# Optimization experiments

Measured on AMD Instinct MI355X. Metric: run time of the kernel, lower is better.

## Reference

```python
import jax, jax.numpy as jnp
import numpy as np

# Dims per init_kwargs
B, C_IN, H, W = 64, 512, 28, 28
GROWTH, BN_SIZE = 32, 4
C_MID = BN_SIZE * GROWTH  # 128
EPS = 1e-5
NUM_BITS = 8          # activation & weight quantization bits
NUM_CHUNKS = 16       # RangeBN chunking (eladhoffer quantize.py default)


def quantize(x, num_bits):
    """Uniform min/max quantize-dequantize (UniformQuantize forward)."""
    mn = x.min()
    mx = x.max()
    qmax = 2.0 ** num_bits - 1.0
    scale = jnp.maximum((mx - mn) / qmax, 1e-8)
    q = jnp.round((jnp.clip(x, mn, mx) - mn) / scale)
    return q * scale + mn


def conv2d(x, w, pad):
    return jax.lax.conv_general_dilated(
        x, w, window_strides=(1, 1), padding=[(pad, pad), (pad, pad)],
        dimension_numbers=('NCHW', 'OIHW', 'NCHW'))


def batchnorm2d(x, w, b):
    # training-mode BN: batch statistics over (N,H,W), biased variance
    mean = x.mean(axis=(0, 2, 3), keepdims=True)
    var = x.var(axis=(0, 2, 3), keepdims=True)
    xhat = (x - mean) * jax.lax.rsqrt(var + EPS)
    return xhat * w.reshape(1, -1, 1, 1) + b.reshape(1, -1, 1, 1)


def range_bn(x, w, b):
    # Range-based BN (training-mode): per-channel mean, scale from chunked min/max range
    Bx, Cx, Hx, Wx = x.shape
    y = x.transpose(1, 0, 2, 3).reshape(Cx, NUM_CHUNKS, -1)  # [C, chunks, n]
    mean_max = y.max(-1).mean(-1)   # [C]
    mean_min = y.min(-1).mean(-1)   # [C]
    mean = y.reshape(Cx, -1).mean(-1)  # [C]
    n = y.shape[-1]
    scale_fix = (0.5 * 0.35) * (1.0 + (np.pi * np.log(4.0)) ** 0.5) / ((2.0 * np.log(float(n))) ** 0.5)
    scale = 1.0 / ((mean_max - mean_min) * scale_fix + EPS)
    out = (x - mean.reshape(1, Cx, 1, 1)) * scale.reshape(1, Cx, 1, 1)
    qw = quantize(w, NUM_BITS)
    qb = quantize(b, NUM_BITS)
    return out * qw.reshape(1, Cx, 1, 1) + qb.reshape(1, Cx, 1, 1)


def setup_inputs() -> dict:
    key = jax.random.key(0)
    ks = jax.random.split(key, 7)
    x = jax.random.normal(ks[0], (B, C_IN, H, W), dtype=jnp.float32)
    bn1_w = jax.random.uniform(ks[1], (C_IN,), dtype=jnp.float32, minval=0.5, maxval=1.5)
    bn1_b = jax.random.normal(ks[2], (C_IN,), dtype=jnp.float32) * 0.1
    conv1_w = jax.random.normal(ks[3], (C_MID, C_IN, 1, 1), dtype=jnp.float32) * (2.0 / C_IN) ** 0.5
    rbn_w = jax.random.uniform(ks[4], (C_MID,), dtype=jnp.float32, minval=0.5, maxval=1.5)
    rbn_b = jax.random.normal(ks[5], (C_MID,), dtype=jnp.float32) * 0.1
    conv2_w = jax.random.normal(ks[6], (GROWTH, C_MID, 3, 3), dtype=jnp.float32) * (2.0 / (9 * C_MID)) ** 0.5
    return {"x": x, "bn1_w": bn1_w, "bn1_b": bn1_b, "conv1_w": conv1_w,
            "rbn_w": rbn_w, "rbn_b": rbn_b, "conv2_w": conv2_w}


def reference(x, bn1_w, bn1_b, conv1_w, rbn_w, rbn_b, conv2_w):
    # norm1 -> relu1 -> QConv2d(1x1) -> RangeBN -> relu2 -> QConv2d(3x3) -> concat
    h = jax.nn.relu(batchnorm2d(x, bn1_w, bn1_b))
    h = conv2d(quantize(h, NUM_BITS), quantize(conv1_w, NUM_BITS), pad=0)
    h = jax.nn.relu(range_bn(h, rbn_w, rbn_b))
    h = conv2d(quantize(h, NUM_BITS), quantize(conv2_w, NUM_BITS), pad=1)
    # drop_rate = 0 -> dropout is identity
    return jnp.concatenate([x, h], axis=1)
```

## Files before the change

### kernel.cpp

```cpp
#include <hip/hip_runtime.h>
#include <math.h>

static constexpr int BB    = 64;
static constexpr int C_IN  = 512;
static constexpr int C_MID = 128;
static constexpr int C_OUT = 32;
static constexpr int C_TOT = 544;
static constexpr int HW    = 784;

static constexpr size_t H2_OFF    = 0;
static constexpr size_t QW1_OFF   = 6422528;
static constexpr size_t QW2_OFF   = QW1_OFF + 65536;
static constexpr size_t PSTAT_OFF = QW2_OFF + 49152;
static constexpr size_t BNA_OFF   = PSTAT_OFF + 16384;
static constexpr size_t BNB_OFF   = BNA_OFF + 512;
static constexpr size_t CMAX_OFF  = BNB_OFF + 512;
static constexpr size_t CMIN_OFF  = CMAX_OFF + 2048;
static constexpr size_t CSUM_OFF  = CMIN_OFF + 2048;
static constexpr size_t A2_OFF    = CSUM_OFF + 2048;
static constexpr size_t B2_OFF    = A2_OFF + 128;
static constexpr size_t QRW_OFF   = B2_OFF + 128;
static constexpr size_t QRB_OFF   = QRW_OFF + 128;
static constexpr size_t SCAL_OFF  = QRB_OFF + 128;
static constexpr size_t PART_OFF  = SCAL_OFF + 16;

#define DEVFN __device__ __forceinline__

typedef __bf16 bf16x8 __attribute__((ext_vector_type(8)));
typedef float  f32x4  __attribute__((ext_vector_type(4)));

DEVFN float qact(float v, float mn, float mx, float inv, float sc) {
    v = fminf(fmaxf(v, mn), mx);
    return fmaf(rintf((v - mn) * inv), sc, mn);
}

DEVFN unsigned f2bf(float f) {
    unsigned u = __float_as_uint(f);
    return (u + 0x7fffu + ((u >> 16) & 1u)) >> 16;
}

__global__ __launch_bounds__(256) void k_stats_copy(const float* __restrict__ x,
                                                    float* __restrict__ out,
                                                    float* __restrict__ ws) {
    const int c = blockIdx.x, bg = blockIdx.y, tid = threadIdx.x;
    float s = 0.f, s2 = 0.f, mn = INFINITY, mx = -INFINITY;
    for (int i = tid; i < 8 * 196; i += 256) {
        const int b = bg * 8 + i / 196, j = i % 196;
        const float4 v = ((const float4*)(x + ((size_t)b * C_IN + c) * HW))[j];
        ((float4*)(out + ((size_t)b * C_TOT + c) * HW))[j] = v;
        s  += (v.x + v.y) + (v.z + v.w);
        s2 += v.x * v.x + v.y * v.y + v.z * v.z + v.w * v.w;
        mn = fminf(mn, fminf(fminf(v.x, v.y), fminf(v.z, v.w)));
        mx = fmaxf(mx, fmaxf(fmaxf(v.x, v.y), fmaxf(v.z, v.w)));
    }
    __shared__ float r0[256], r1[256], r2[256], r3[256];
    r0[tid] = s; r1[tid] = s2; r2[tid] = mn; r3[tid] = mx;
    __syncthreads();
    for (int off = 128; off > 0; off >>= 1) {
        if (tid < off) {
            r0[tid] += r0[tid + off];
            r1[tid] += r1[tid + off];
            r2[tid] = fminf(r2[tid], r2[tid + off]);
            r3[tid] = fmaxf(r3[tid], r3[tid + off]);
        }
        __syncthreads();
    }
    if (tid == 0) {
        float* p = ws + PSTAT_OFF + ((size_t)c * 8 + bg) * 4;
        p[0] = r0[0]; p[1] = r1[0]; p[2] = r2[0]; p[3] = r3[0];
    }
}

__global__ __launch_bounds__(256) void k_prep_red(const float* __restrict__ conv1_w,
                                                  const float* __restrict__ conv2_w,
                                                  const float* __restrict__ bn1_w,
                                                  const float* __restrict__ bn1_b,
                                                  float* __restrict__ ws) {
    const int b = blockIdx.x, tid = threadIdx.x;
    __shared__ float ra[256], rb[256];
    float mn = INFINITY, mx = -INFINITY;

    if (b < 32) {
        const float4* src = (const float4*)conv1_w + (size_t)b * 512;
        for (int i = tid; i < 512; i += 256) {
            const float4 v = src[i];
            mn = fminf(mn, fminf(fminf(v.x, v.y), fminf(v.z, v.w)));
            mx = fmaxf(mx, fmaxf(fmaxf(v.x, v.y), fmaxf(v.z, v.w)));
        }
    } else if (b < 40) {
        const float4* src = (const float4*)conv2_w + (size_t)(b - 32) * 1152;
        for (int i = tid; i < 1152; i += 256) {
            const float4 v = src[i];
            mn = fminf(mn, fminf(fminf(v.x, v.y), fminf(v.z, v.w)));
            mx = fmaxf(mx, fmaxf(fmaxf(v.x, v.y), fmaxf(v.z, v.w)));
        }
    } else {
        if (tid < 128) {
            const int c = (b - 40) * 128 + tid;
            const float* p = ws + PSTAT_OFF + (size_t)c * 32;
            float s = 0.f, s2 = 0.f, cmn = INFINITY, cmx = -INFINITY;
            for (int g = 0; g < 8; ++g) {
                s += p[g * 4 + 0]; s2 += p[g * 4 + 1];
                cmn = fminf(cmn, p[g * 4 + 2]); cmx = fmaxf(cmx, p[g * 4 + 3]);
            }
            const float n = 50176.f;
            const float mean = s / n;
            const float var  = s2 / n - mean * mean;
            const float rstd = rsqrtf(var + 1e-5f);
            const float A  = rstd * bn1_w[c];
            const float Bc = bn1_b[c] - mean * A;
            ws[BNA_OFF + c] = A; ws[BNB_OFF + c] = Bc;
            const float v1 = A * cmn + Bc, v2 = A * cmx + Bc;
            mn = fmaxf(0.f, fminf(v1, v2));
            mx = fmaxf(0.f, fmaxf(v1, v2));
        }
    }
    ra[tid] = mn; rb[tid] = mx;
    __syncthreads();
    for (int off = 128; off > 0; off >>= 1) {
        if (tid < off) { ra[tid] = fminf(ra[tid], ra[tid + off]); rb[tid] = fmaxf(rb[tid], rb[tid + off]); }
        __syncthreads();
    }
    if (tid == 0) {
        float* p;
        if (b < 32)       p = ws + PART_OFF + (size_t)b * 2;
        else if (b < 40)  p = ws + PART_OFF + 64 + (size_t)(b - 32) * 2;
        else              p = ws + PART_OFF + 80 + (size_t)(b - 40) * 2;
        p[0] = ra[0]; p[1] = rb[0];
    }
}

__global__ __launch_bounds__(256) void k_prep_fin(const float* __restrict__ rbn_w,
                                                  const float* __restrict__ rbn_b,
                                                  float* __restrict__ ws) {
    const int tid = threadIdx.x;
    __shared__ float ra[256], rb[256];
    __shared__ float s_mn, s_sc;

    ra[tid] = tid < 32 ? ws[PART_OFF + tid * 2] : INFINITY;
    rb[tid] = tid < 32 ? ws[PART_OFF + tid * 2 + 1] : -INFINITY;
    __syncthreads();
    for (int off = 128; off > 0; off >>= 1) {
        if (tid < off) { ra[tid] = fminf(ra[tid], ra[tid + off]); rb[tid] = fmaxf(rb[tid], rb[tid + off]); }
        __syncthreads();
    }
    if (tid == 0) {
        ws[SCAL_OFF + 8] = ra[0];
        ws[SCAL_OFF + 9] = fmaxf((rb[0] - ra[0]) / 255.f, 1e-8f);
    }
    __syncthreads();

    ra[tid] = tid < 8 ? ws[PART_OFF + 64 + tid * 2] : INFINITY;
    rb[tid] = tid < 8 ? ws[PART_OFF + 64 + tid * 2 + 1] : -INFINITY;
    __syncthreads();
    for (int off = 128; off > 0; off >>= 1) {
        if (tid < off) { ra[tid] = fminf(ra[tid], ra[tid + off]); rb[tid] = fmaxf(rb[tid], rb[tid + off]); }
        __syncthreads();
    }
    if (tid == 0) {
        ws[SCAL_OFF + 10] = ra[0];
        ws[SCAL_OFF + 11] = fmaxf((rb[0] - ra[0]) / 255.f, 1e-8f);
    }
    __syncthreads();

    ra[tid] = tid < 4 ? ws[PART_OFF + 80 + tid * 2] : INFINITY;
    rb[tid] = tid < 4 ? ws[PART_OFF + 80 + tid * 2 + 1] : -INFINITY;
    __syncthreads();
    for (int off = 128; off > 0; off >>= 1) {
        if (tid < off) { ra[tid] = fminf(ra[tid], ra[tid + off]); rb[tid] = fmaxf(rb[tid], rb[tid + off]); }
        __syncthreads();
    }
    if (tid == 0) {
        const float mn1 = ra[0], mx1 = rb[0];
        const float sc = fmaxf((mx1 - mn1) / 255.f, 1e-8f);
        ws[SCAL_OFF + 0] = mn1; ws[SCAL_OFF + 1] = sc; ws[SCAL_OFF + 2] = 1.f / sc; ws[SCAL_OFF + 6] = mx1;
    }
    __syncthreads();

    for (int which = 0; which < 2; ++which) {
        const float* src = which ? rbn_b : rbn_w;
        const size_t dst = which ? QRB_OFF : QRW_OFF;
        float v = 0.f;
        ra[tid] = INFINITY; rb[tid] = -INFINITY;
        if (tid < 128) { v = src[tid]; ra[tid] = v; rb[tid] = v; }
        __syncthreads();
        for (int off = 128; off > 0; off >>= 1) {
            if (tid < off) { ra[tid] = fminf(ra[tid], ra[tid + off]); rb[tid] = fmaxf(rb[tid], rb[tid + off]); }
            __syncthreads();
        }
        if (tid == 0) { s_mn = ra[0]; s_sc = fmaxf((rb[0] - ra[0]) / 255.f, 1e-8f); }
        __syncthreads();
        if (tid < 128) ws[dst + tid] = fmaf(rintf((v - s_mn) / s_sc), s_sc, s_mn);
        __syncthreads();
    }
}

__global__ __launch_bounds__(256) void k_prep_quant(const float* __restrict__ conv1_w,
                                                    const float* __restrict__ conv2_w,
                                                    float* __restrict__ ws) {
    const int b = blockIdx.x, tid = threadIdx.x;
    if (b < 32) {
        const float mnw = ws[SCAL_OFF + 8], scw = ws[SCAL_OFF + 9];
        unsigned short* qw = (unsigned short*)(ws + QW1_OFF);
        const int base = b * 2048;
#pragma unroll
        for (int t = 0; t < 8; ++t) {
            const int i = base + t * 256 + tid;
            const int co = i >> 9, k = i & 511;
            const float v = conv1_w[i];
            const float qv = fmaf(rintf((v - mnw) / scw), scw, mnw);
            const int ks = k >> 6, kc = (k >> 3) & 7, klo = k & 7;
            qw[(((size_t)ks * 128 + co) << 6) + (((kc ^ (co & 7)) << 3) | klo)] = (unsigned short)f2bf(qv);
        }
    } else {
        const float mnw = ws[SCAL_OFF + 10], scw = ws[SCAL_OFF + 11];
        unsigned short* qw2 = (unsigned short*)(ws + QW2_OFF);
        const int base = (b - 32) * 4608;
        for (int i2 = tid; i2 < 4608; i2 += 256) {
            const int i = base + i2;
            const int co = i / 1152, r = i % 1152, ci = r / 9, tap = r % 9;
            const float v = conv2_w[i];
            const float qv = fmaf(rintf((v - mnw) / scw), scw, mnw);
            qw2[(size_t)co * 1152 + tap * 128 + ci] = (unsigned short)f2bf(qv);
        }
    }
}

__global__ __launch_bounds__(256, 2) void k_conv1(const float* __restrict__ x, float* __restrict__ ws) {
    __shared__ __align__(16) unsigned short wt[128 * 64];
    __shared__ __align__(16) unsigned short ht[112 * 64];
    const int tid = threadIdx.x;
    const int pt = blockIdx.x, b = blockIdx.y;
    const int p0 = pt * 112;
    const float mn1 = ws[SCAL_OFF + 0], sc1 = ws[SCAL_OFF + 1];
    const float inv1 = ws[SCAL_OFF + 2], mx1 = ws[SCAL_OFF + 6];
    const unsigned short* qw1 = (const unsigned short*)(ws + QW1_OFF);
    const float* xb = x + (size_t)b * C_IN * HW;

    const int o = tid & 7, q = tid >> 3;
    const int wv = tid >> 6, g = (tid >> 4) & 3, r4 = tid & 15;

    f32x4 acc[2][7];
#pragma unroll
    for (int i = 0; i < 2; ++i)
#pragma unroll
        for (int j = 0; j < 7; ++j) acc[i][j] = f32x4{0.f, 0.f, 0.f, 0.f};

    for (int ks = 0; ks < 8; ++ks) {
        const float4* wsrc = (const float4*)(qw1 + (size_t)ks * 8192);
        float4* wdst = (float4*)wt;
#pragma unroll
        for (int i = 0; i < 4; ++i) wdst[tid + i * 256] = wsrc[tid + i * 256];

        if (tid < 224) {
            const int ci0 = ks * 64 + o * 8;
            float vv[8][4];
#pragma unroll
            for (int j = 0; j < 8; ++j) {
                const float4 v = *(const float4*)(xb + (size_t)(ci0 + j) * HW + p0 + q * 4);
                const float A = ws[BNA_OFF + ci0 + j], Bc = ws[BNB_OFF + ci0 + j];
                vv[j][0] = qact(fmaxf(0.f, fmaf(v.x, A, Bc)), mn1, mx1, inv1, sc1);
                vv[j][1] = qact(fmaxf(0.f, fmaf(v.y, A, Bc)), mn1, mx1, inv1, sc1);
                vv[j][2] = qact(fmaxf(0.f, fmaf(v.z, A, Bc)), mn1, mx1, inv1, sc1);
                vv[j][3] = qact(fmaxf(0.f, fmaf(v.w, A, Bc)), mn1, mx1, inv1, sc1);
            }
#pragma unroll
            for (int r = 0; r < 4; ++r) {
                const int p = q * 4 + r;
                uint4 pk;
                pk.x = f2bf(vv[0][r]) | (f2bf(vv[1][r]) << 16);
                pk.y = f2bf(vv[2][r]) | (f2bf(vv[3][r]) << 16);
                pk.z = f2bf(vv[4][r]) | (f2bf(vv[5][r]) << 16);
                pk.w = f2bf(vv[6][r]) | (f2bf(vv[7][r]) << 16);
                *(uint4*)&ht[p * 64 + ((o ^ (p & 7)) << 3)] = pk;
            }
        }
        __syncthreads();

#pragma unroll
        for (int ksub = 0; ksub < 2; ++ksub) {
            const int kk = ksub * 4 + g;
            bf16x8 af[2], bfr[7];
#pragma unroll
            for (int ct = 0; ct < 2; ++ct) {
                const int co = wv * 32 + ct * 16 + r4;
                af[ct] = *(const bf16x8*)&wt[co * 64 + ((kk ^ (co & 7)) << 3)];
            }
#pragma unroll
            for (int pf = 0; pf < 7; ++pf) {
                const int p = pf * 16 + r4;
                bfr[pf] = *(const bf16x8*)&ht[p * 64 + ((kk ^ (p & 7)) << 3)];
            }
#pragma unroll
            for (int ct = 0; ct < 2; ++ct)
#pragma unroll
                for (int pf = 0; pf < 7; ++pf)
                    acc[ct][pf] = __builtin_amdgcn_mfma_f32_16x16x32_bf16(af[ct], bfr[pf], acc[ct][pf], 0, 0, 0);
        }
        __syncthreads();
    }

    float* hb = ws + H2_OFF + (size_t)b * C_MID * HW;
#pragma unroll
    for (int ct = 0; ct < 2; ++ct) {
        const int co0 = wv * 32 + ct * 16 + g * 4;
#pragma unroll
        for (int pf = 0; pf < 7; ++pf) {
            const int p = p0 + pf * 16 + r4;
#pragma unroll
            for (int r = 0; r < 4; ++r)
                hb[(size_t)(co0 + r) * HW + p] = acc[ct][pf][r];
        }
    }
}

__global__ __launch_bounds__(256) void k_rbn_stats(float* __restrict__ ws) {
    const int c = blockIdx.x, ch = blockIdx.y, tid = threadIdx.x;
    float s = 0.f, mn = INFINITY, mx = -INFINITY;
    for (int i = tid; i < 784; i += 256) {
        const int b = ch * 4 + i / 196, j = i % 196;
        const float4 v = ((const float4*)(ws + H2_OFF + ((size_t)b * C_MID + c) * HW))[j];
        s += (v.x + v.y) + (v.z + v.w);
        mn = fminf(mn, fminf(fminf(v.x, v.y), fminf(v.z, v.w)));
        mx = fmaxf(mx, fmaxf(fmaxf(v.x, v.y), fmaxf(v.z, v.w)));
    }
    __shared__ float r0[256], r1[256], r2[256];
    r0[tid] = s; r1[tid] = mn; r2[tid] = mx;
    __syncthreads();
    for (int off = 128; off > 0; off >>= 1) {
        if (tid < off) {
            r0[tid] += r0[tid + off];
            r1[tid] = fminf(r1[tid], r1[tid + off]);
            r2[tid] = fmaxf(r2[tid], r2[tid + off]);
        }
        __syncthreads();
    }
    if (tid == 0) {
        ws[CSUM_OFF + (size_t)c * 16 + ch] = r0[0];
        ws[CMIN_OFF + (size_t)c * 16 + ch] = r1[0];
        ws[CMAX_OFF + (size_t)c * 16 + ch] = r2[0];
    }
}

__global__ __launch_bounds__(256) void k_prep2(float* __restrict__ ws) {
    const int tid = threadIdx.x;
    __shared__ float ra[256], rb[256];
    float lo = INFINITY, hi = -INFINITY;
    if (tid < 128) {
        const int c = tid;
        float mm = 0.f, mnm = 0.f, s = 0.f, cmx = -INFINITY, cmn = INFINITY;
        for (int ch = 0; ch < 16; ++ch) {
            const float a = ws[CMAX_OFF + (size_t)c * 16 + ch];
            const float m = ws[CMIN_OFF + (size_t)c * 16 + ch];
            mm += a; mnm += m; s += ws[CSUM_OFF + (size_t)c * 16 + ch];
            cmx = fmaxf(cmx, a); cmn = fminf(cmn, m);
        }
        mm *= (1.f / 16.f); mnm *= (1.f / 16.f);
        const float mean = s / 50176.f;
        const double PI_D = 3.14159265358979323846;
        const double sfd = 0.175 * (1.0 + sqrt(PI_D * log(4.0))) / sqrt(2.0 * log(3136.0));
        const float scale = 1.f / ((mm - mnm) * (float)sfd + 1e-5f);
        const float A  = scale * ws[QRW_OFF + c];
        const float Bc = ws[QRB_OFF + c] - mean * A;
        ws[A2_OFF + c] = A; ws[B2_OFF + c] = Bc;
        const float v1 = A * cmn + Bc, v2 = A * cmx + Bc;
        lo = fmaxf(0.f, fminf(v1, v2));
        hi = fmaxf(0.f, fmaxf(v1, v2));
    }
    ra[tid] = lo; rb[tid] = hi;
    __syncthreads();
    for (int off = 128; off > 0; off >>= 1) {
        if (tid < off) { ra[tid] = fminf(ra[tid], ra[tid + off]); rb[tid] = fmaxf(rb[tid], rb[tid + off]); }
        __syncthreads();
    }
    if (tid == 0) {
        const float mn3 = ra[0], mx3 = rb[0];
        const float sc = fmaxf((mx3 - mn3) / 255.f, 1e-8f);
        ws[SCAL_OFF + 3] = mn3; ws[SCAL_OFF + 4] = sc; ws[SCAL_OFF + 5] = 1.f / sc; ws[SCAL_OFF + 7] = mx3;
    }
}

__global__ __launch_bounds__(128) void k_conv2(float* __restrict__ out, const float* __restrict__ ws) {
    __shared__ __align__(16) unsigned short lact[7 * 30 * 128];
    const int tid = threadIdx.x;
    const int pt = blockIdx.x, b = blockIdx.y;
    const int y0 = pt * 4;
    const float mn3 = ws[SCAL_OFF + 3], sc3 = ws[SCAL_OFF + 4];
    const float inv3 = ws[SCAL_OFF + 5], mx3 = ws[SCAL_OFF + 7];

    {
        const uint4 z = {0u, 0u, 0u, 0u};
        uint4* lp = (uint4*)lact;
        for (int i = tid; i < 3360; i += 128) lp[i] = z;
    }
    __syncthreads();

    const float* h2b = ws + H2_OFF + (size_t)b * C_MID * HW;
    for (int task = tid; task < 672; task += 128) {
        const int oct = task / 42, rem = task % 42, r = rem / 7, xq = rem % 7;
        const int gy = y0 - 1 + r;
        if (gy < 0 || gy > 27) continue;
        float vv[8][4];
#pragma unroll
        for (int j = 0; j < 8; ++j) {
            const int ci = oct * 8 + j;
            const float4 v = *(const float4*)(h2b + (size_t)ci * HW + gy * 28 + xq * 4);
            const float A = ws[A2_OFF + ci], Bc = ws[B2_OFF + ci];
            vv[j][0] = qact(fmaxf(0.f, fmaf(v.x, A, Bc)), mn3, mx3, inv3, sc3);
            vv[j][1] = qact(fmaxf(0.f, fmaf(v.y, A, Bc)), mn3, mx3, inv3, sc3);
            vv[j][2] = qact(fmaxf(0.f, fmaf(v.z, A, Bc)), mn3, mx3, inv3, sc3);
            vv[j][3] = qact(fmaxf(0.f, fmaf(v.w, A, Bc)), mn3, mx3, inv3, sc3);
        }
#pragma unroll
        for (int xi = 0; xi < 4; ++xi) {
            const int col = xq * 4 + xi + 1;
            const int phys = (oct + col) & 15;
            uint4 pk;
            pk.x = f2bf(vv[0][xi]) | (f2bf(vv[1][xi]) << 16);
            pk.y = f2bf(vv[2][xi]) | (f2bf(vv[3][xi]) << 16);
            pk.z = f2bf(vv[4][xi]) | (f2bf(vv[5][xi]) << 16);
            pk.w = f2bf(vv[6][xi]) | (f2bf(vv[7][xi]) << 16);
            *(uint4*)&lact[((r * 30 + col) * 16 + phys) * 8] = pk;
        }
    }
    __syncthreads();

    const int wv = tid >> 6, lane = tid & 63, r4 = lane & 15, g = lane >> 4;
    int py[4], px[4];
#pragma unroll
    for (int i = 0; i < 4; ++i) {
        const int p = (wv * 4 + i) * 16 + r4;
        py[i] = p / 28; px[i] = p % 28;
    }
    f32x4 acc[2][4];
#pragma unroll
    for (int ct = 0; ct < 2; ++ct)
#pragma unroll
        for (int i = 0; i < 4; ++i) acc[ct][i] = f32x4{0.f, 0.f, 0.f, 0.f};

    const unsigned short* qw2 = (const unsigned short*)(ws + QW2_OFF);
    for (int tap = 0; tap < 9; ++tap) {
        const int dy = tap / 3, dx = tap % 3;
        bf16x8 afr[2][4];
#pragma unroll
        for (int ct = 0; ct < 2; ++ct)
#pragma unroll
            for (int c4 = 0; c4 < 4; ++c4) {
                const int co = ct * 16 + r4;
                afr[ct][c4] = *(const bf16x8*)&qw2[(size_t)co * 1152 + tap * 128 + c4 * 32 + g * 8];
            }
#pragma unroll
        for (int c4 = 0; c4 < 4; ++c4) {
            bf16x8 bfr[4];
#pragma unroll
            for (int i = 0; i < 4; ++i) {
                const int row = py[i] + dy, col = px[i] + dx;
                const int phys = (c4 * 4 + g + col) & 15;
                bfr[i] = *(const bf16x8*)&lact[((row * 30 + col) * 16 + phys) * 8];
            }
#pragma unroll
            for (int ct = 0; ct < 2; ++ct)
#pragma unroll
                for (int i = 0; i < 4; ++i)
                    acc[ct][i] = __builtin_amdgcn_mfma_f32_16x16x32_bf16(afr[ct][c4], bfr[i], acc[ct][i], 0, 0, 0);
        }
    }

#pragma unroll
    for (int ct = 0; ct < 2; ++ct)
#pragma unroll
        for (int i = 0; i < 4; ++i) {
            const int pf = wv * 4 + i;
            if (pf < 7) {
                const int p = pf * 16 + r4;
#pragma unroll
                for (int r = 0; r < 4; ++r) {
                    const int co = ct * 16 + g * 4 + r;
                    out[((size_t)b * C_TOT + 512 + co) * HW + y0 * 28 + p] = acc[ct][i][r];
                }
            }
        }
}

extern "C" void kernel_launch(void* const* d_in, const int* in_sizes, int n_in,
                              void* d_out, int out_size, void* d_ws, size_t ws_size,
                              hipStream_t stream) {
    const float* x       = (const float*)d_in[0];
    const float* bn1_w   = (const float*)d_in[1];
    const float* bn1_b   = (const float*)d_in[2];
    const float* conv1_w = (const float*)d_in[3];
    const float* rbn_w   = (const float*)d_in[4];
    const float* rbn_b   = (const float*)d_in[5];
    const float* conv2_w = (const float*)d_in[6];
    float* out = (float*)d_out;
    float* ws  = (float*)d_ws;

    k_stats_copy<<<dim3(512, 8), 256, 0, stream>>>(x, out, ws);
    k_prep_red<<<44, 256, 0, stream>>>(conv1_w, conv2_w, bn1_w, bn1_b, ws);
    k_prep_fin<<<1, 256, 0, stream>>>(rbn_w, rbn_b, ws);
    k_prep_quant<<<40, 256, 0, stream>>>(conv1_w, conv2_w, ws);
    k_conv1<<<dim3(7, 64), 256, 0, stream>>>(x, ws);
    k_rbn_stats<<<dim3(128, 16), 256, 0, stream>>>(ws);
    k_prep2<<<1, 256, 0, stream>>>(ws);
    k_conv2<<<dim3(7, 64), 128, 0, stream>>>(out, ws);
}
```

Measured before the change: 111.7 us.

## Fuse passthrough copy and RangeBN stats into conv1 epilogue

```diff
diff --git a/kernel.cpp b/kernel.cpp
--- a/kernel.cpp
+++ b/kernel.cpp
@@ -23,6 +23,8 @@
 static constexpr size_t QRB_OFF   = QRW_OFF + 128;
 static constexpr size_t SCAL_OFF  = QRB_OFF + 128;
 static constexpr size_t PART_OFF  = SCAL_OFF + 16;
+static constexpr size_t RP_OFF    = PART_OFF + 128;
+static constexpr size_t PART2_OFF = RP_OFF + 172032;
 
 #define DEVFN __device__ __forceinline__
 
@@ -39,19 +41,21 @@
     return (u + 0x7fffu + ((u >> 16) & 1u)) >> 16;
 }
 
-__global__ __launch_bounds__(256) void k_stats_copy(const float* __restrict__ x,
-                                                    float* __restrict__ out,
-                                                    float* __restrict__ ws) {
+__global__ __launch_bounds__(256) void k_stats(const float* __restrict__ x,
+                                               float* __restrict__ ws) {
     const int c = blockIdx.x, bg = blockIdx.y, tid = threadIdx.x;
     float s = 0.f, s2 = 0.f, mn = INFINITY, mx = -INFINITY;
-    for (int i = tid; i < 8 * 196; i += 256) {
-        const int b = bg * 8 + i / 196, j = i % 196;
-        const float4 v = ((const float4*)(x + ((size_t)b * C_IN + c) * HW))[j];
-        ((float4*)(out + ((size_t)b * C_TOT + c) * HW))[j] = v;
-        s  += (v.x + v.y) + (v.z + v.w);
-        s2 += v.x * v.x + v.y * v.y + v.z * v.z + v.w * v.w;
-        mn = fminf(mn, fminf(fminf(v.x, v.y), fminf(v.z, v.w)));
-        mx = fmaxf(mx, fmaxf(fmaxf(v.x, v.y), fmaxf(v.z, v.w)));
+    if (tid < 224) {
+#pragma unroll
+        for (int k = 0; k < 7; ++k) {
+            const int idx = k * 224 + tid;
+            const int b = bg * 8 + idx / 196, j = idx % 196;
+            const float4 v = ((const float4*)(x + ((size_t)b * C_IN + c) * HW))[j];
+            s  += (v.x + v.y) + (v.z + v.w);
+            s2 += v.x * v.x + v.y * v.y + v.z * v.z + v.w * v.w;
+            mn = fminf(mn, fminf(fminf(v.x, v.y), fminf(v.z, v.w)));
+            mx = fmaxf(mx, fmaxf(fmaxf(v.x, v.y), fmaxf(v.z, v.w)));
+        }
     }
     __shared__ float r0[256], r1[256], r2[256], r3[256];
     r0[tid] = s; r1[tid] = s2; r2[tid] = mn; r3[tid] = mx;
@@ -226,7 +230,9 @@
     }
 }
 
-__global__ __launch_bounds__(256, 2) void k_conv1(const float* __restrict__ x, float* __restrict__ ws) {
+__global__ __launch_bounds__(256, 2) void k_conv1(const float* __restrict__ x,
+                                                  float* __restrict__ out,
+                                                  float* __restrict__ ws) {
     __shared__ __align__(16) unsigned short wt[128 * 64];
     __shared__ __align__(16) unsigned short ht[112 * 64];
     const int tid = threadIdx.x;
@@ -236,6 +242,7 @@
     const float inv1 = ws[SCAL_OFF + 2], mx1 = ws[SCAL_OFF + 6];
     const unsigned short* qw1 = (const unsigned short*)(ws + QW1_OFF);
     const float* xb = x + (size_t)b * C_IN * HW;
+    float* outb = out + (size_t)b * C_TOT * HW;
 
     const int o = tid & 7, q = tid >> 3;
     const int wv = tid >> 6, g = (tid >> 4) & 3, r4 = tid & 15;
@@ -257,7 +264,8 @@
             float vv[8][4];
 #pragma unroll
             for (int j = 0; j < 8; ++j) {
-                const float4 v = *(const float4*)(xb + (size_t)(ci0 + j) * HW + p0 + q * 4);
+                const f32x4 v = *(const f32x4*)(xb + (size_t)(ci0 + j) * HW + p0 + q * 4);
+                __builtin_nontemporal_store(v, (f32x4*)(outb + (size_t)(ci0 + j) * HW + p0 + q * 4));
                 const float A = ws[BNA_OFF + ci0 + j], Bc = ws[BNB_OFF + ci0 + j];
                 vv[j][0] = qact(fmaxf(0.f, fmaf(v.x, A, Bc)), mn1, mx1, inv1, sc1);
                 vv[j][1] = qact(fmaxf(0.f, fmaf(v.y, A, Bc)), mn1, mx1, inv1, sc1);
@@ -312,71 +320,85 @@
                 hb[(size_t)(co0 + r) * HW + p] = acc[ct][pf][r];
         }
     }
-}
-
-__global__ __launch_bounds__(256) void k_rbn_stats(float* __restrict__ ws) {
-    const int c = blockIdx.x, ch = blockIdx.y, tid = threadIdx.x;
+
+#pragma unroll
+    for (int ct = 0; ct < 2; ++ct)
+#pragma unroll
+        for (int r = 0; r < 4; ++r) {
+            float s = 0.f, mn = INFINITY, mx = -INFINITY;
+#pragma unroll
+            for (int pf = 0; pf < 7; ++pf) {
+                const float v = acc[ct][pf][r];
+                s += v; mn = fminf(mn, v); mx = fmaxf(mx, v);
+            }
+#pragma unroll
+            for (int m = 1; m < 16; m <<= 1) {
+                s  += __shfl_xor(s, m, 64);
+                mn  = fminf(mn, __shfl_xor(mn, m, 64));
+                mx  = fmaxf(mx, __shfl_xor(mx, m, 64));
+            }
+            if (r4 == 0) {
+                const int co = wv * 32 + ct * 16 + g * 4 + r;
+                float* dst = ws + RP_OFF + (((size_t)co * 64 + b) * 7 + pt) * 3;
+                dst[0] = s; dst[1] = mn; dst[2] = mx;
+            }
+        }
+}
+
+__global__ __launch_bounds__(64) void k_rbn_combine(float* __restrict__ ws) {
+    const int c = blockIdx.x, t = threadIdx.x;
+    const int ch = t >> 2, sub = t & 3;
+    const int b = ch * 4 + sub;
+    const float* rp = ws + RP_OFF + ((size_t)c * 64 + b) * 21;
     float s = 0.f, mn = INFINITY, mx = -INFINITY;
-    for (int i = tid; i < 784; i += 256) {
-        const int b = ch * 4 + i / 196, j = i % 196;
-        const float4 v = ((const float4*)(ws + H2_OFF + ((size_t)b * C_MID + c) * HW))[j];
-        s += (v.x + v.y) + (v.z + v.w);
-        mn = fminf(mn, fminf(fminf(v.x, v.y), fminf(v.z, v.w)));
-        mx = fmaxf(mx, fmaxf(fmaxf(v.x, v.y), fmaxf(v.z, v.w)));
-    }
-    __shared__ float r0[256], r1[256], r2[256];
-    r0[tid] = s; r1[tid] = mn; r2[tid] = mx;
-    __syncthreads();
-    for (int off = 128; off > 0; off >>= 1) {
-        if (tid < off) {
-            r0[tid] += r0[tid + off];
-            r1[tid] = fminf(r1[tid], r1[tid + off]);
-            r2[tid] = fmaxf(r2[tid], r2[tid + off]);
-        }
-        __syncthreads();
-    }
-    if (tid == 0) {
-        ws[CSUM_OFF + (size_t)c * 16 + ch] = r0[0];
-        ws[CMIN_OFF + (size_t)c * 16 + ch] = r1[0];
-        ws[CMAX_OFF + (size_t)c * 16 + ch] = r2[0];
-    }
-}
-
-__global__ __launch_bounds__(256) void k_prep2(float* __restrict__ ws) {
-    const int tid = threadIdx.x;
-    __shared__ float ra[256], rb[256];
-    float lo = INFINITY, hi = -INFINITY;
-    if (tid < 128) {
-        const int c = tid;
-        float mm = 0.f, mnm = 0.f, s = 0.f, cmx = -INFINITY, cmn = INFINITY;
-        for (int ch = 0; ch < 16; ++ch) {
-            const float a = ws[CMAX_OFF + (size_t)c * 16 + ch];
-            const float m = ws[CMIN_OFF + (size_t)c * 16 + ch];
-            mm += a; mnm += m; s += ws[CSUM_OFF + (size_t)c * 16 + ch];
-            cmx = fmaxf(cmx, a); cmn = fminf(cmn, m);
-        }
-        mm *= (1.f / 16.f); mnm *= (1.f / 16.f);
-        const float mean = s / 50176.f;
+#pragma unroll
+    for (int pt = 0; pt < 7; ++pt) {
+        s += rp[pt * 3 + 0];
+        mn = fminf(mn, rp[pt * 3 + 1]);
+        mx = fmaxf(mx, rp[pt * 3 + 2]);
+    }
+#pragma unroll
+    for (int m = 1; m < 4; m <<= 1) {
+        s  += __shfl_xor(s, m, 64);
+        mn  = fminf(mn, __shfl_xor(mn, m, 64));
+        mx  = fmaxf(mx, __shfl_xor(mx, m, 64));
+    }
+    float smx = mx, smn = mn, stot = s, gmn = mn, gmx = mx;
+#pragma unroll
+    for (int m = 4; m < 64; m <<= 1) {
+        smx  += __shfl_xor(smx, m, 64);
+        smn  += __shfl_xor(smn, m, 64);
+        stot += __shfl_xor(stot, m, 64);
+        gmn   = fminf(gmn, __shfl_xor(gmn, m, 64));
+        gmx   = fmaxf(gmx, __shfl_xor(gmx, m, 64));
+    }
+    if (t == 0) {
+        const float mm = smx * (1.f / 16.f), mnm = smn * (1.f / 16.f);
+        const float mean = stot / 50176.f;
         const double PI_D = 3.14159265358979323846;
         const double sfd = 0.175 * (1.0 + sqrt(PI_D * log(4.0))) / sqrt(2.0 * log(3136.0));
         const float scale = 1.f / ((mm - mnm) * (float)sfd + 1e-5f);
         const float A  = scale * ws[QRW_OFF + c];
         const float Bc = ws[QRB_OFF + c] - mean * A;
         ws[A2_OFF + c] = A; ws[B2_OFF + c] = Bc;
-        const float v1 = A * cmn + Bc, v2 = A * cmx + Bc;
-        lo = fmaxf(0.f, fminf(v1, v2));
-        hi = fmaxf(0.f, fmaxf(v1, v2));
-    }
-    ra[tid] = lo; rb[tid] = hi;
-    __syncthreads();
-    for (int off = 128; off > 0; off >>= 1) {
-        if (tid < off) { ra[tid] = fminf(ra[tid], ra[tid + off]); rb[tid] = fmaxf(rb[tid], rb[tid + off]); }
-        __syncthreads();
-    }
-    if (tid == 0) {
-        const float mn3 = ra[0], mx3 = rb[0];
-        const float sc = fmaxf((mx3 - mn3) / 255.f, 1e-8f);
-        ws[SCAL_OFF + 3] = mn3; ws[SCAL_OFF + 4] = sc; ws[SCAL_OFF + 5] = 1.f / sc; ws[SCAL_OFF + 7] = mx3;
+        const float v1 = A * gmn + Bc, v2 = A * gmx + Bc;
+        ws[PART2_OFF + c * 2 + 0] = fmaxf(0.f, fminf(v1, v2));
+        ws[PART2_OFF + c * 2 + 1] = fmaxf(0.f, fmaxf(v1, v2));
+    }
+}
+
+__global__ __launch_bounds__(64) void k_prep2b(float* __restrict__ ws) {
+    const int t = threadIdx.x;
+    float lo = fminf(ws[PART2_OFF + t * 2], ws[PART2_OFF + (t + 64) * 2]);
+    float hi = fmaxf(ws[PART2_OFF + t * 2 + 1], ws[PART2_OFF + (t + 64) * 2 + 1]);
+#pragma unroll
+    for (int m = 1; m < 64; m <<= 1) {
+        lo = fminf(lo, __shfl_xor(lo, m, 64));
+        hi = fmaxf(hi, __shfl_xor(hi, m, 64));
+    }
+    if (t == 0) {
+        const float sc = fmaxf((hi - lo) / 255.f, 1e-8f);
+        ws[SCAL_OFF + 3] = lo; ws[SCAL_OFF + 4] = sc; ws[SCAL_OFF + 5] = 1.f / sc; ws[SCAL_OFF + 7] = hi;
     }
 }
 
@@ -495,12 +517,12 @@
     float* out = (float*)d_out;
     float* ws  = (float*)d_ws;
 
-    k_stats_copy<<<dim3(512, 8), 256, 0, stream>>>(x, out, ws);
+    k_stats<<<dim3(512, 8), 256, 0, stream>>>(x, ws);
     k_prep_red<<<44, 256, 0, stream>>>(conv1_w, conv2_w, bn1_w, bn1_b, ws);
     k_prep_fin<<<1, 256, 0, stream>>>(rbn_w, rbn_b, ws);
     k_prep_quant<<<40, 256, 0, stream>>>(conv1_w, conv2_w, ws);
-    k_conv1<<<dim3(7, 64), 256, 0, stream>>>(x, ws);
-    k_rbn_stats<<<dim3(128, 16), 256, 0, stream>>>(ws);
-    k_prep2<<<1, 256, 0, stream>>>(ws);
+    k_conv1<<<dim3(7, 64), 256, 0, stream>>>(x, out, ws);
+    k_rbn_combine<<<128, 64, 0, stream>>>(ws);
+    k_prep2b<<<1, 64, 0, stream>>>(ws);
     k_conv2<<<dim3(7, 64), 128, 0, stream>>>(out, ws);
 }
```

Measured after the change: 106.1 us. 5.0% less time.
